# Kernel optimization log

Measured on AMD Instinct MI355X. Metric: run time of the kernel, lower is better.

Reference implementation:

```python
import jax, jax.numpy as jnp
import numpy as np

N, E, HDIM, NG = 10000, 320000, 256, 20
BN_EPS = 1e-5


def setup_inputs() -> dict:
    key = jax.random.key(0)
    ks = jax.random.split(key, 12)
    inp = {
        "x": jax.random.normal(ks[0], (N, HDIM), dtype=jnp.float32),
        "rbf": jax.random.uniform(ks[1], (E, NG), dtype=jnp.float32),
        "ei": jax.random.randint(ks[2], (2, E), 0, N, dtype=jnp.int64),
        # filter_net: Linear(n_g, hdim) -> SiLU -> Linear(hdim, hdim)
        "Wf1": jax.random.normal(ks[3], (NG, HDIM), dtype=jnp.float32) / np.sqrt(NG),
        "bf1": jnp.zeros((HDIM,), dtype=jnp.float32),
        "Wf2": jax.random.normal(ks[4], (HDIM, HDIM), dtype=jnp.float32) / np.sqrt(HDIM),
        "bf2": jnp.zeros((HDIM,), dtype=jnp.float32),
        # node_update: Linear(hdim, hdim) -> SiLU -> Linear(hdim, hdim)
        "Wu1": jax.random.normal(ks[5], (HDIM, HDIM), dtype=jnp.float32) / np.sqrt(HDIM),
        "bu1": jnp.zeros((HDIM,), dtype=jnp.float32),
        "Wu2": jax.random.normal(ks[6], (HDIM, HDIM), dtype=jnp.float32) / np.sqrt(HDIM),
        "bu2": jnp.zeros((HDIM,), dtype=jnp.float32),
        # BatchNorm1d affine params
        "gamma": jnp.ones((HDIM,), dtype=jnp.float32),
        "beta": jnp.zeros((HDIM,), dtype=jnp.float32),
    }
    return inp


def reference(x, rbf, Wf1, bf1, Wf2, bf2, Wu1, bu1, Wu2, bu2, gamma, beta, ei):
    row, col = ei[0], ei[1]
    # filter_net(rbf): [E, hdim]
    filt = jax.nn.silu(rbf @ Wf1 + bf1) @ Wf2 + bf2
    # message = gather(x, col) * filter
    msg = x[col] * filt  # [E, hdim]
    # scatter_add aggregation over destination nodes
    agg = jax.ops.segment_sum(msg, row, num_segments=x.shape[0])  # [N, hdim]
    # node_update MLP
    h = jax.nn.silu(agg @ Wu1 + bu1) @ Wu2 + bu2  # [N, hdim]
    # BatchNorm1d (training mode: batch stats, biased variance)
    mean = jnp.mean(h, axis=0)
    var = jnp.mean(jnp.square(h - mean), axis=0)
    bn = gamma * (h - mean) * jax.lax.rsqrt(var + BN_EPS) + beta
    return x + bn
```

## Files before the change

### kernel.cpp

```cpp
#include <hip/hip_runtime.h>

#define N_NODES 10000
#define E_EDGES 320000
#define HDIM    256
#define NG      20
#define BN_EPS  1e-5f

typedef __attribute__((ext_vector_type(8))) short short8;
typedef __attribute__((ext_vector_type(4))) float f32x4;

__device__ __forceinline__ float silu_f(float v) {
    float e = __expf(-v);
    return v * __builtin_amdgcn_rcpf(1.0f + e);
}

__device__ __forceinline__ unsigned int cvt_pk(float lo, float hi) {
    unsigned int r;
    asm("v_cvt_pk_bf16_f32 %0, %1, %2" : "=v"(r) : "v"(lo), "v"(hi));
    return r;
}

__device__ __forceinline__ unsigned short f2bf(float f) {
    union { float f; unsigned int u; } v; v.f = f;
    unsigned int r = v.u + 0x7fffu + ((v.u >> 16) & 1u);
    return (unsigned short)(r >> 16);
}

__device__ __forceinline__ f32x4 bf4_to_f32(uint2 u) {
    union { unsigned int i; float f; } a, b, c, d;
    a.i = u.x << 16; b.i = u.x & 0xFFFF0000u;
    c.i = u.y << 16; d.i = u.y & 0xFFFF0000u;
    return (f32x4){a.f, b.f, c.f, d.f};
}

__global__ __launch_bounds__(256) void prep_hist_kernel(
    const float* __restrict__ Wf2, const float* __restrict__ Wu1,
    const float* __restrict__ Wu2, const float* __restrict__ Wf1,
    const float* __restrict__ bf1, const int* __restrict__ ei_row,
    const float* __restrict__ x,
    unsigned short* __restrict__ Pf2, unsigned short* __restrict__ Pu1,
    unsigned short* __restrict__ Pu2, unsigned short* __restrict__ P1,
    int* __restrict__ cnt, unsigned short* __restrict__ xb)
{
    const int bx = blockIdx.x;
    if (bx >= 2050) {
        const int idx = ((bx - 2050) * 256 + threadIdx.x) * 8;
        const float4* s = (const float4*)(x + idx);
        float4 a = s[0], b = s[1];
        *(uint4*)(xb + idx) = make_uint4(cvt_pk(a.x, a.y), cvt_pk(a.z, a.w),
                                         cvt_pk(b.x, b.y), cvt_pk(b.z, b.w));
        return;
    }
    if (bx >= 800) {
        int e = (bx - 800) * 256 + threadIdx.x;
        atomicAdd(&cnt[ei_row[e]], 1);
        return;
    }
    int tid = bx * 256 + threadIdx.x;
    if (tid < 196608) {
        int which = tid >> 16, local = tid & 65535;
        const float* W = (which == 0) ? Wf2 : (which == 1) ? Wu1 : Wu2;
        unsigned short* P = (which == 0) ? Pf2 : (which == 1) ? Pu1 : Pu2;
        int j = local & 7, lane = (local >> 3) & 63;
        int ntile = (local >> 9) & 15, kstep = local >> 13;
        int k = kstep * 32 + (lane >> 4) * 8 + j;
        int n = ntile * 16 + (lane & 15);
        P[local] = f2bf(W[k * 256 + n]);
    } else {
        int local = tid - 196608;
        int j = local & 7, lane = (local >> 3) & 63, ntile = local >> 9;
        int k = (lane >> 4) * 8 + j;
        int n = ntile * 16 + (lane & 15);
        float v = (k < NG) ? Wf1[k * 256 + n] : (k == NG ? bf1[n] : 0.0f);
        P1[local] = f2bf(v);
    }
}

__global__ __launch_bounds__(256) void scan_kernel(int* __restrict__ cnt) {
    __shared__ int tot[256];
    const int t = threadIdx.x;
    int loc[40];
    int s = 0;
    #pragma unroll
    for (int i = 0; i < 40; ++i) { loc[i] = cnt[t * 40 + i]; s += loc[i]; }
    tot[t] = s;
    __syncthreads();
    for (int off = 1; off < 256; off <<= 1) {
        int u = (t >= off) ? tot[t - off] : 0;
        __syncthreads();
        tot[t] += u;
        __syncthreads();
    }
    int pre = tot[t] - s;
    #pragma unroll
    for (int i = 0; i < 40; ++i) { int v = loc[i]; cnt[t * 40 + i] = pre; pre += v; }
}

__global__ __launch_bounds__(256) void fill_kernel(const int* __restrict__ ei_row,
                                                   const int* __restrict__ ei_col,
                                                   int* __restrict__ cnt,
                                                   int* __restrict__ perm,
                                                   int* __restrict__ nodepos,
                                                   int* __restrict__ colperm) {
    int e = blockIdx.x * 256 + threadIdx.x;
    int r = ei_row[e];
    int c = ei_col[e];
    int pos = atomicAdd(&cnt[r], 1);
    perm[pos] = e;
    nodepos[pos] = r;
    colperm[pos] = c;
}

#define SM_NID 0
#define SM_RBF 256
#define SM_HID 5376
#define SM_TOT 38144

__global__ __launch_bounds__(512, 6) void edge_kernel(
    const float* __restrict__ rbf, const int* __restrict__ perm,
    const int* __restrict__ nodepos, const int* __restrict__ colperm,
    const unsigned short* __restrict__ P1, const unsigned short* __restrict__ P2,
    const float* __restrict__ bf2, const unsigned short* __restrict__ xb,
    float* __restrict__ agg)
{
    __shared__ char sm[SM_TOT];
    int* nid_s = (int*)(sm + SM_NID);

    const int t = threadIdx.x;
    int blk = blockIdx.x;
    blk = (blk & 7) * 625 + (blk >> 3);
    const int p0 = blk * 64;
    const int l = t & 63, w = t >> 6;
    const int l15 = l & 15, l4 = l >> 4;

    if (t < 64) nid_s[t] = nodepos[p0 + t];
    if (t < 128) {
        const int row = t >> 1, half = t & 1;
        const float* rp = rbf + (size_t)perm[p0 + row] * NG + half * 10;
        float v[10];
        if (half == 0) {
            float4 a = *(const float4*)rp, b = *(const float4*)(rp + 4);
            float2 c = *(const float2*)(rp + 8);
            v[0]=a.x; v[1]=a.y; v[2]=a.z; v[3]=a.w; v[4]=b.x;
            v[5]=b.y; v[6]=b.z; v[7]=b.w; v[8]=c.x; v[9]=c.y;
        } else {
            float2 a = *(const float2*)rp;
            float4 b = *(const float4*)(rp + 2), c = *(const float4*)(rp + 6);
            v[0]=a.x; v[1]=a.y; v[2]=b.x; v[3]=b.y; v[4]=b.z;
            v[5]=b.w; v[6]=c.x; v[7]=c.y; v[8]=c.z; v[9]=c.w;
        }
        unsigned int* dst = (unsigned int*)(sm + SM_RBF + row * 80 + half * 20);
        #pragma unroll
        for (int i = 0; i < 5; ++i) dst[i] = cvt_pk(v[2*i], v[2*i+1]);
    } else if (t < 192) {
        const int row = t - 128;
        *(unsigned long long*)(sm + SM_RBF + row * 80 + 40) = 0x3F80ull;
        *(uint4*)(sm + SM_RBF + row * 80 + 48) = make_uint4(0, 0, 0, 0);
    }

    int colp[4];
    #pragma unroll
    for (int nt = 0; nt < 4; ++nt) colp[nt] = colperm[p0 + nt * 16 + l15];

    short8 a1[2], acur[2];
    #pragma unroll
    for (int mt = 0; mt < 2; ++mt) {
        a1[mt]   = *(const short8*)(P1 + ((2 * w + mt) * 64 + l) * 8);
        acur[mt] = *(const short8*)(P2 + ((2 * w + mt) * 64 + l) * 8);
    }

    __syncthreads();

    f32x4 acc[2][4];
    #pragma unroll
    for (int mt = 0; mt < 2; ++mt)
        #pragma unroll
        for (int nt = 0; nt < 4; ++nt) acc[mt][nt] = (f32x4)0.0f;

    #pragma unroll
    for (int nt = 0; nt < 4; ++nt) {
        short8 bfr = *(const short8*)(sm + SM_RBF + (nt * 16 + l15) * 80 + l4 * 16);
        #pragma unroll
        for (int mt = 0; mt < 2; ++mt)
            acc[mt][nt] = __builtin_amdgcn_mfma_f32_16x16x32_bf16(a1[mt], bfr, acc[mt][nt], 0, 0, 0);
    }

    #pragma unroll
    for (int mt = 0; mt < 2; ++mt) {
        const int hc0 = w * 32 + mt * 16 + l4 * 4;
        #pragma unroll
        for (int nt = 0; nt < 4; ++nt) {
            const int row = nt * 16 + l15;
            unsigned int pk0 = cvt_pk(silu_f(acc[mt][nt][0]), silu_f(acc[mt][nt][1]));
            unsigned int pk1 = cvt_pk(silu_f(acc[mt][nt][2]), silu_f(acc[mt][nt][3]));
            *(uint2*)(sm + SM_HID + row * 512 +
                      (((hc0 >> 3) ^ (row & 7)) << 4) + (hc0 & 7) * 2) =
                make_uint2(pk0, pk1);
        }
    }
    __syncthreads();

    #pragma unroll
    for (int mt = 0; mt < 2; ++mt)
        #pragma unroll
        for (int nt = 0; nt < 4; ++nt) acc[mt][nt] = (f32x4)0.0f;

    for (int ks = 0; ks < 8; ++ks) {
        short8 anext[2];
        if (ks < 7) {
            #pragma unroll
            for (int mt = 0; mt < 2; ++mt)
                anext[mt] = *(const short8*)(P2 + (((ks + 1) * 16 + 2 * w + mt) * 64 + l) * 8);
        }
        #pragma unroll
        for (int nt = 0; nt < 4; ++nt) {
            const int row = nt * 16 + l15;
            short8 bfh = *(const short8*)(sm + SM_HID + row * 512 +
                            ((((ks << 2) + l4) ^ (row & 7)) << 4));
            #pragma unroll
            for (int mt = 0; mt < 2; ++mt)
                acc[mt][nt] = __builtin_amdgcn_mfma_f32_16x16x32_bf16(acur[mt], bfh, acc[mt][nt], 0, 0, 0);
        }
        if (ks < 7) {
            #pragma unroll
            for (int mt = 0; mt < 2; ++mt) acur[mt] = anext[mt];
        }
    }

    uint2 xv[2][4];
    #pragma unroll
    for (int mt = 0; mt < 2; ++mt) {
        const int fc0 = w * 32 + mt * 16 + l4 * 4;
        #pragma unroll
        for (int nt = 0; nt < 4; ++nt)
            xv[mt][nt] = *(const uint2*)(xb + (size_t)colp[nt] * HDIM + fc0);
    }

    f32x4 bc2[2];
    #pragma unroll
    for (int mt = 0; mt < 2; ++mt)
        bc2[mt] = *(const f32x4*)(bf2 + w * 32 + mt * 16 + l4 * 4);

    __syncthreads();

    #pragma unroll
    for (int mt = 0; mt < 2; ++mt) {
        const int fc0 = w * 32 + mt * 16 + l4 * 4;
        #pragma unroll
        for (int nt = 0; nt < 4; ++nt) {
            const int row = nt * 16 + l15;
            f32x4 m = (acc[mt][nt] + bc2[mt]) * bf4_to_f32(xv[mt][nt]);
            *(uint2*)(sm + SM_HID + row * 512 +
                      (((fc0 >> 3) ^ (row & 7)) << 4) + (fc0 & 7) * 2) =
                make_uint2(cvt_pk(m[0], m[1]), cvt_pk(m[2], m[3]));
        }
    }
    __syncthreads();

    if (t < 256) {
        float sum = 0.0f;
        int cur = nid_s[0];
        for (int pos = 0; pos < 64; ++pos) {
            const int nid = nid_s[pos];
            unsigned short u = *(const unsigned short*)(sm + SM_HID + pos * 512 +
                                (((t >> 3) ^ (pos & 7)) << 4) + (t & 7) * 2);
            union { unsigned int i; float f; } cv; cv.i = ((unsigned int)u) << 16;
            if (nid != cur) {
                atomicAdd(&agg[(size_t)cur * HDIM + t], sum);
                sum = 0.0f; cur = nid;
            }
            sum += cv.f;
        }
        atomicAdd(&agg[(size_t)cur * HDIM + t], sum);
    }
}

__global__ __launch_bounds__(256, 3) void node_kernel(
    const float* __restrict__ agg, const float* __restrict__ bu1,
    const float* __restrict__ bu2,
    const unsigned short* __restrict__ Pu1, const unsigned short* __restrict__ Pu2,
    float* __restrict__ hout, float* __restrict__ sums)
{
    __shared__ char sm[32768];
    const int t  = threadIdx.x;
    const int r0 = blockIdx.x * 64;
    const int l = t & 63, w = t >> 6;
    const int l15 = l & 15, l4 = l >> 4;

    {
        const int row = t & 63, q = t >> 6;
        const bool valid = (r0 + row) < N_NODES;
        const float4* src = (const float4*)(agg + (size_t)(r0 + row) * HDIM) + q * 16;
        #pragma unroll
        for (int i = 0; i < 16; ++i) {
            float4 v = valid ? src[i] : make_float4(0.f, 0.f, 0.f, 0.f);
            const int c0 = q * 64 + i * 4;
            *(uint2*)(sm + row * 512 + (((c0 >> 3) ^ (row & 7)) << 4) + (c0 & 7) * 2) =
                make_uint2(cvt_pk(v.x, v.y), cvt_pk(v.z, v.w));
        }
    }

    short8 acur[4];
    #pragma unroll
    for (int mt = 0; mt < 4; ++mt)
        acur[mt] = *(const short8*)(Pu1 + ((4 * w + mt) * 64 + l) * 8);

    __syncthreads();

    f32x4 acc[4][4];
    #pragma unroll
    for (int mt = 0; mt < 4; ++mt)
        #pragma unroll
        for (int nt = 0; nt < 4; ++nt) acc[mt][nt] = (f32x4)0.0f;

    for (int ks = 0; ks < 8; ++ks) {
        short8 anext[4];
        if (ks < 7) {
            #pragma unroll
            for (int mt = 0; mt < 4; ++mt)
                anext[mt] = *(const short8*)(Pu1 + (((ks + 1) * 16 + 4 * w + mt) * 64 + l) * 8);
        }
        #pragma unroll
        for (int nt = 0; nt < 4; ++nt) {
            const int row = nt * 16 + l15;
            short8 bfa = *(const short8*)(sm + row * 512 +
                            ((((ks << 2) + l4) ^ (row & 7)) << 4));
            #pragma unroll
            for (int mt = 0; mt < 4; ++mt)
                acc[mt][nt] = __builtin_amdgcn_mfma_f32_16x16x32_bf16(acur[mt], bfa, acc[mt][nt], 0, 0, 0);
        }
        if (ks < 7) {
            #pragma unroll
            for (int mt = 0; mt < 4; ++mt) acur[mt] = anext[mt];
        }
    }
    __syncthreads();

    #pragma unroll
    for (int mt = 0; mt < 4; ++mt)
        acur[mt] = *(const short8*)(Pu2 + ((4 * w + mt) * 64 + l) * 8);

    #pragma unroll
    for (int mt = 0; mt < 4; ++mt) {
        const int mc0 = w * 64 + mt * 16 + l4 * 4;
        f32x4 b4 = *(const f32x4*)(bu1 + mc0);
        #pragma unroll
        for (int nt = 0; nt < 4; ++nt) {
            const int row = nt * 16 + l15;
            unsigned int pk0 = cvt_pk(silu_f(acc[mt][nt][0] + b4[0]), silu_f(acc[mt][nt][1] + b4[1]));
            unsigned int pk1 = cvt_pk(silu_f(acc[mt][nt][2] + b4[2]), silu_f(acc[mt][nt][3] + b4[3]));
            *(uint2*)(sm + row * 512 + (((mc0 >> 3) ^ (row & 7)) << 4) + (mc0 & 7) * 2) =
                make_uint2(pk0, pk1);
            acc[mt][nt] = (f32x4)0.0f;
        }
    }
    __syncthreads();

    for (int ks = 0; ks < 8; ++ks) {
        short8 anext[4];
        if (ks < 7) {
            #pragma unroll
            for (int mt = 0; mt < 4; ++mt)
                anext[mt] = *(const short8*)(Pu2 + (((ks + 1) * 16 + 4 * w + mt) * 64 + l) * 8);
        }
        #pragma unroll
        for (int nt = 0; nt < 4; ++nt) {
            const int row = nt * 16 + l15;
            short8 bfm = *(const short8*)(sm + row * 512 +
                            ((((ks << 2) + l4) ^ (row & 7)) << 4));
            #pragma unroll
            for (int mt = 0; mt < 4; ++mt)
                acc[mt][nt] = __builtin_amdgcn_mfma_f32_16x16x32_bf16(acur[mt], bfm, acc[mt][nt], 0, 0, 0);
        }
        if (ks < 7) {
            #pragma unroll
            for (int mt = 0; mt < 4; ++mt) acur[mt] = anext[mt];
        }
    }

    #pragma unroll
    for (int mt = 0; mt < 4; ++mt) {
        const int hc0 = w * 64 + mt * 16 + l4 * 4;
        f32x4 b4 = *(const f32x4*)(bu2 + hc0);
        f32x4 s = (f32x4)0.0f, s2 = (f32x4)0.0f;
        #pragma unroll
        for (int nt = 0; nt < 4; ++nt) {
            const int gr = r0 + nt * 16 + l15;
            if (gr < N_NODES) {
                f32x4 hv = acc[mt][nt] + b4;
                *(f32x4*)(hout + (size_t)gr * HDIM + hc0) = hv;
                s += hv; s2 += hv * hv;
            }
        }
        #pragma unroll
        for (int off = 1; off < 16; off <<= 1) {
            #pragma unroll
            for (int r = 0; r < 4; ++r) {
                s[r]  += __shfl_xor(s[r], off);
                s2[r] += __shfl_xor(s2[r], off);
            }
        }
        if (l15 == 0) {
            #pragma unroll
            for (int r = 0; r < 4; ++r) {
                atomicAdd(&sums[hc0 + r], s[r]);
                atomicAdd(&sums[HDIM + hc0 + r], s2[r]);
            }
        }
    }
}

__global__ __launch_bounds__(256) void final_kernel(
    const float* __restrict__ x, const float* __restrict__ sums,
    const float* __restrict__ gamma, const float* __restrict__ beta,
    float* __restrict__ out)
{
    const int i4 = blockIdx.x * 256 + threadIdx.x;
    const int j  = (i4 & 63) * 4;
    f32x4 mean = *(const f32x4*)(sums + j) * (1.0f / N_NODES);
    f32x4 s2   = *(const f32x4*)(sums + HDIM + j) * (1.0f / N_NODES);
    f32x4 g    = *(const f32x4*)(gamma + j);
    f32x4 b    = *(const f32x4*)(beta + j);
    f32x4 hv   = ((f32x4*)out)[i4];
    f32x4 xv   = ((const f32x4*)x)[i4];
    f32x4 var  = s2 - mean * mean;
    f32x4 inv;
    #pragma unroll
    for (int r = 0; r < 4; ++r) inv[r] = rsqrtf(var[r] + BN_EPS);
    ((f32x4*)out)[i4] = xv + g * (hv - mean) * inv + b;
}

extern "C" void kernel_launch(void* const* d_in, const int* in_sizes, int n_in,
                              void* d_out, int out_size, void* d_ws, size_t ws_size,
                              hipStream_t stream) {
    const float* x     = (const float*)d_in[0];
    const float* rbf   = (const float*)d_in[1];
    const int*   ei    = (const int*)d_in[2];
    const float* Wf1   = (const float*)d_in[3];
    const float* bf1   = (const float*)d_in[4];
    const float* Wf2   = (const float*)d_in[5];
    const float* bf2   = (const float*)d_in[6];
    const float* Wu1   = (const float*)d_in[7];
    const float* bu1   = (const float*)d_in[8];
    const float* Wu2   = (const float*)d_in[9];
    const float* bu2   = (const float*)d_in[10];
    const float* gamma = (const float*)d_in[11];
    const float* beta  = (const float*)d_in[12];
    float* out = (float*)d_out;

    char* ws = (char*)d_ws;
    float* agg     = (float*)(ws);
    float* sums    = (float*)(ws + 10240000);
    int*   cnt     = (int*)(ws + 10242048);
    int*   perm    = (int*)(ws + 10283008);
    int*   nodepos = (int*)(ws + 11563008);
    unsigned short* Pf2 = (unsigned short*)(ws + 12843008);
    unsigned short* Pu1 = (unsigned short*)(ws + 12974080);
    unsigned short* Pu2 = (unsigned short*)(ws + 13105152);
    unsigned short* P1  = (unsigned short*)(ws + 13236224);

    unsigned short* xb = (unsigned short*)d_out;
    int* colperm = (int*)((char*)d_out + 5120000);

    hipMemsetAsync(agg, 0, 10283008, stream);

    prep_hist_kernel<<<3300, 256, 0, stream>>>(Wf2, Wu1, Wu2, Wf1, bf1, ei, x,
                                               Pf2, Pu1, Pu2, P1, cnt, xb);
    scan_kernel<<<1, 256, 0, stream>>>(cnt);
    fill_kernel<<<E_EDGES / 256, 256, 0, stream>>>(ei, ei + E_EDGES, cnt,
                                                   perm, nodepos, colperm);

    edge_kernel<<<E_EDGES / 64, 512, 0, stream>>>(
        rbf, perm, nodepos, colperm, P1, Pf2, bf2, xb, agg);
    node_kernel<<<(N_NODES + 63) / 64, 256, 0, stream>>>(
        agg, bu1, bu2, Pu1, Pu2, out, sums);
    final_kernel<<<(N_NODES * HDIM / 4) / 256, 256, 0, stream>>>(
        x, sums, gamma, beta, out);
}
```

Measured before the change: 199.1 us.

## Split edge segment reduction across both thread halves and widen node kernel to 512 threads

The edge kernel's final per-column segmented reduction over 64 sorted edges now uses all 512 threads: each half reduces 32 edges. Boundary partial sums are stitched through shared memory so a segment that spans both halves issues one combined atomic. Loads are batched eight at a time to raise ILP. The node MLP kernel moves from 256 to 512 threads per block with half the output tiles per wave, lowering registers per thread and adding waves to hide latency, at the cost of more blocks' worth of synchronization and weight loads per block.

```diff
diff --git a/kernel.cpp b/kernel.cpp
--- a/kernel.cpp
+++ b/kernel.cpp
@@ -257,25 +257,60 @@
     }
     __syncthreads();
 
-    if (t < 256) {
+    {
+        const int col = t & 255;
+        const int h   = t >> 8;
+        const int base = h * 32;
+        int* stash_nid   = (int*)(sm + SM_RBF);
+        float* stash_sum = (float*)(sm + SM_RBF + 1024);
+
         float sum = 0.0f;
-        int cur = nid_s[0];
-        for (int pos = 0; pos < 64; ++pos) {
-            const int nid = nid_s[pos];
-            unsigned short u = *(const unsigned short*)(sm + SM_HID + pos * 512 +
-                                (((t >> 3) ^ (pos & 7)) << 4) + (t & 7) * 2);
-            union { unsigned int i; float f; } cv; cv.i = ((unsigned int)u) << 16;
-            if (nid != cur) {
-                atomicAdd(&agg[(size_t)cur * HDIM + t], sum);
-                sum = 0.0f; cur = nid;
+        int cur = nid_s[base];
+        int fnid = 0; float fsum = 0.0f;
+        bool held = false;
+
+        #pragma unroll
+        for (int c = 0; c < 4; ++c) {
+            float v[8];
+            #pragma unroll
+            for (int i = 0; i < 8; ++i) {
+                const int pos = base + c * 8 + i;
+                unsigned short u = *(const unsigned short*)(sm + SM_HID + pos * 512 +
+                                    (((col >> 3) ^ (pos & 7)) << 4) + (col & 7) * 2);
+                union { unsigned int ii; float f; } cv; cv.ii = ((unsigned int)u) << 16;
+                v[i] = cv.f;
             }
-            sum += cv.f;
-        }
-        atomicAdd(&agg[(size_t)cur * HDIM + t], sum);
-    }
-}
-
-__global__ __launch_bounds__(256, 3) void node_kernel(
+            #pragma unroll
+            for (int i = 0; i < 8; ++i) {
+                const int nid = nid_s[base + c * 8 + i];
+                if (nid != cur) {
+                    if (h == 1 && !held) { fnid = cur; fsum = sum; held = true; }
+                    else atomicAdd(&agg[(size_t)cur * HDIM + col], sum);
+                    sum = 0.0f; cur = nid;
+                }
+                sum += v[i];
+            }
+        }
+        if (h == 0) {
+            stash_nid[col] = cur; stash_sum[col] = sum;
+        } else {
+            if (!held) { fnid = cur; fsum = sum; }
+            else atomicAdd(&agg[(size_t)cur * HDIM + col], sum);
+        }
+        __syncthreads();
+        if (h == 1) {
+            int n0 = stash_nid[col]; float s0 = stash_sum[col];
+            if (n0 == fnid) {
+                atomicAdd(&agg[(size_t)n0 * HDIM + col], s0 + fsum);
+            } else {
+                atomicAdd(&agg[(size_t)n0 * HDIM + col], s0);
+                atomicAdd(&agg[(size_t)fnid * HDIM + col], fsum);
+            }
+        }
+    }
+}
+
+__global__ __launch_bounds__(512, 2) void node_kernel(
     const float* __restrict__ agg, const float* __restrict__ bu1,
     const float* __restrict__ bu2,
     const unsigned short* __restrict__ Pu1, const unsigned short* __restrict__ Pu2,
@@ -290,35 +325,35 @@
     {
         const int row = t & 63, q = t >> 6;
         const bool valid = (r0 + row) < N_NODES;
-        const float4* src = (const float4*)(agg + (size_t)(r0 + row) * HDIM) + q * 16;
-        #pragma unroll
-        for (int i = 0; i < 16; ++i) {
+        const float4* src = (const float4*)(agg + (size_t)(r0 + row) * HDIM) + q * 8;
+        #pragma unroll
+        for (int i = 0; i < 8; ++i) {
             float4 v = valid ? src[i] : make_float4(0.f, 0.f, 0.f, 0.f);
-            const int c0 = q * 64 + i * 4;
+            const int c0 = q * 32 + i * 4;
             *(uint2*)(sm + row * 512 + (((c0 >> 3) ^ (row & 7)) << 4) + (c0 & 7) * 2) =
                 make_uint2(cvt_pk(v.x, v.y), cvt_pk(v.z, v.w));
         }
     }
 
-    short8 acur[4];
-    #pragma unroll
-    for (int mt = 0; mt < 4; ++mt)
-        acur[mt] = *(const short8*)(Pu1 + ((4 * w + mt) * 64 + l) * 8);
-
-    __syncthreads();
-
-    f32x4 acc[4][4];
-    #pragma unroll
-    for (int mt = 0; mt < 4; ++mt)
+    short8 acur[2];
+    #pragma unroll
+    for (int mt = 0; mt < 2; ++mt)
+        acur[mt] = *(const short8*)(Pu1 + ((2 * w + mt) * 64 + l) * 8);
+
+    __syncthreads();
+
+    f32x4 acc[2][4];
+    #pragma unroll
+    for (int mt = 0; mt < 2; ++mt)
         #pragma unroll
         for (int nt = 0; nt < 4; ++nt) acc[mt][nt] = (f32x4)0.0f;
 
     for (int ks = 0; ks < 8; ++ks) {
-        short8 anext[4];
+        short8 anext[2];
         if (ks < 7) {
             #pragma unroll
-            for (int mt = 0; mt < 4; ++mt)
-                anext[mt] = *(const short8*)(Pu1 + (((ks + 1) * 16 + 4 * w + mt) * 64 + l) * 8);
+            for (int mt = 0; mt < 2; ++mt)
+                anext[mt] = *(const short8*)(Pu1 + (((ks + 1) * 16 + 2 * w + mt) * 64 + l) * 8);
         }
         #pragma unroll
         for (int nt = 0; nt < 4; ++nt) {
@@ -326,23 +361,23 @@
             short8 bfa = *(const short8*)(sm + row * 512 +
                             ((((ks << 2) + l4) ^ (row & 7)) << 4));
             #pragma unroll
-            for (int mt = 0; mt < 4; ++mt)
+            for (int mt = 0; mt < 2; ++mt)
                 acc[mt][nt] = __builtin_amdgcn_mfma_f32_16x16x32_bf16(acur[mt], bfa, acc[mt][nt], 0, 0, 0);
         }
         if (ks < 7) {
             #pragma unroll
-            for (int mt = 0; mt < 4; ++mt) acur[mt] = anext[mt];
-        }
-    }
-    __syncthreads();
-
-    #pragma unroll
-    for (int mt = 0; mt < 4; ++mt)
-        acur[mt] = *(const short8*)(Pu2 + ((4 * w + mt) * 64 + l) * 8);
-
-    #pragma unroll
-    for (int mt = 0; mt < 4; ++mt) {
-        const int mc0 = w * 64 + mt * 16 + l4 * 4;
+            for (int mt = 0; mt < 2; ++mt) acur[mt] = anext[mt];
+        }
+    }
+    __syncthreads();
+
+    #pragma unroll
+    for (int mt = 0; mt < 2; ++mt)
+        acur[mt] = *(const short8*)(Pu2 + ((2 * w + mt) * 64 + l) * 8);
+
+    #pragma unroll
+    for (int mt = 0; mt < 2; ++mt) {
+        const int mc0 = w * 32 + mt * 16 + l4 * 4;
         f32x4 b4 = *(const f32x4*)(bu1 + mc0);
         #pragma unroll
         for (int nt = 0; nt < 4; ++nt) {
@@ -357,11 +392,11 @@
     __syncthreads();
 
     for (int ks = 0; ks < 8; ++ks) {
-        short8 anext[4];
+        short8 anext[2];
         if (ks < 7) {
             #pragma unroll
-            for (int mt = 0; mt < 4; ++mt)
-                anext[mt] = *(const short8*)(Pu2 + (((ks + 1) * 16 + 4 * w + mt) * 64 + l) * 8);
+            for (int mt = 0; mt < 2; ++mt)
+                anext[mt] = *(const short8*)(Pu2 + (((ks + 1) * 16 + 2 * w + mt) * 64 + l) * 8);
         }
         #pragma unroll
         for (int nt = 0; nt < 4; ++nt) {
@@ -369,18 +404,18 @@
             short8 bfm = *(const short8*)(sm + row * 512 +
                             ((((ks << 2) + l4) ^ (row & 7)) << 4));
             #pragma unroll
-            for (int mt = 0; mt < 4; ++mt)
+            for (int mt = 0; mt < 2; ++mt)
                 acc[mt][nt] = __builtin_amdgcn_mfma_f32_16x16x32_bf16(acur[mt], bfm, acc[mt][nt], 0, 0, 0);
         }
         if (ks < 7) {
             #pragma unroll
-            for (int mt = 0; mt < 4; ++mt) acur[mt] = anext[mt];
-        }
-    }
-
-    #pragma unroll
-    for (int mt = 0; mt < 4; ++mt) {
-        const int hc0 = w * 64 + mt * 16 + l4 * 4;
+            for (int mt = 0; mt < 2; ++mt) acur[mt] = anext[mt];
+        }
+    }
+
+    #pragma unroll
+    for (int mt = 0; mt < 2; ++mt) {
+        const int hc0 = w * 32 + mt * 16 + l4 * 4;
         f32x4 b4 = *(const f32x4*)(bu2 + hc0);
         f32x4 s = (f32x4)0.0f, s2 = (f32x4)0.0f;
         #pragma unroll
@@ -472,7 +507,7 @@
 
     edge_kernel<<<E_EDGES / 64, 512, 0, stream>>>(
         rbf, perm, nodepos, colperm, P1, Pf2, bf2, xb, agg);
-    node_kernel<<<(N_NODES + 63) / 64, 256, 0, stream>>>(
+    node_kernel<<<(N_NODES + 63) / 64, 512, 0, stream>>>(
         agg, bu1, bu2, Pu1, Pu2, out, sums);
     final_kernel<<<(N_NODES * HDIM / 4) / 256, 256, 0, stream>>>(
         x, sums, gamma, beta, out);
```

After: 184.0 us. -7.6%, faster.
